# Kernel optimization log

Hardware: AMD Instinct MI355X
Metric: run time of the kernel (lower is better)

## Reference

```python
import jax, jax.numpy as jnp
import numpy as np

U, I, E, T = 60000, 30000, 64, 2000
N = U + I
ADJ_NNZ = 1_600_000
UI_NNZ = 800_000
TAGS_PER_ITEM = 4


def setup_inputs() -> dict:
    key = jax.random.key(0)
    ks = jax.random.split(key, 8)
    # LightGCN normalized adjacency in COO form (values already normalized offline)
    adj_rows = jax.random.randint(ks[0], (ADJ_NNZ,), 0, N, dtype=jnp.int32)
    adj_cols = jax.random.randint(ks[1], (ADJ_NNZ,), 0, N, dtype=jnp.int32)
    adj_vals = jax.random.uniform(ks[2], (ADJ_NNZ,), dtype=jnp.float32) * 0.01
    # Item-tag incidence H: 4 distinct tags per item (binary incidence, no duplicates)
    items_np = np.repeat(np.arange(I, dtype=np.int32), TAGS_PER_ITEM)
    tags_np = ((np.arange(I, dtype=np.int64)[:, None] * 7919 + np.arange(TAGS_PER_ITEM)[None, :] * 131) % T).astype(np.int32).reshape(-1)
    h_items = jnp.asarray(items_np)
    h_tags = jnp.asarray(tags_np)
    # Row-normalized user-item interaction matrix (D_u^-1 @ trn_mat) in COO form
    ui_rows = jax.random.randint(ks[3], (UI_NNZ,), 0, U, dtype=jnp.int32)
    ui_cols = jax.random.randint(ks[4], (UI_NNZ,), 0, I, dtype=jnp.int32)
    ui_vals = jax.random.uniform(ks[5], (UI_NNZ,), dtype=jnp.float32) * 0.01
    return {
        'user_embeds': jax.random.normal(ks[6], (U, E), dtype=jnp.float32) * 0.1,
        'item_embeds': jax.random.normal(jax.random.fold_in(ks[6], 1), (I, E), dtype=jnp.float32) * 0.1,
        'hypergraph_user_embeds': jax.random.normal(ks[7], (U, E), dtype=jnp.float32) * 0.1,
        'hypergraph_item_embeds': jax.random.normal(jax.random.fold_in(ks[7], 1), (I, E), dtype=jnp.float32) * 0.1,
        'adj_rows': adj_rows, 'adj_cols': adj_cols, 'adj_vals': adj_vals,
        'h_items': h_items, 'h_tags': h_tags,
        'ui_rows': ui_rows, 'ui_cols': ui_cols, 'ui_vals': ui_vals,
        'layer_num': 3,
    }


def _spmm(rows, cols, vals, x, n):
    # y[r] += vals[e] * x[cols[e]] for each edge e with rows[e]==r  (t.spmm)
    return jax.ops.segment_sum(vals[:, None] * x[cols], rows, num_segments=n)


def reference(user_embeds, item_embeds, hypergraph_user_embeds, hypergraph_item_embeds,
              adj_rows, adj_cols, adj_vals, h_items, h_tags, ui_rows, ui_cols, ui_vals,
              layer_num):
    ones = jnp.ones(h_items.shape[0], dtype=user_embeds.dtype)
    # B: hyperedge (tag) degree; D: item degree; zero degrees clamped to 1
    B = jax.ops.segment_sum(ones, h_tags, num_segments=T)
    D = jax.ops.segment_sum(ones, h_items, num_segments=I)
    B_inv = 1.0 / jnp.where(B == 0, 1.0, B)
    D_inv = 1.0 / jnp.where(D == 0, 1.0, D)

    def hconv(x):  # D^-1 H B^-1 H^T x, never materializing the item x item adjacency
        y = jax.ops.segment_sum(x[h_items], h_tags, num_segments=T) * B_inv[:, None]
        z = jax.ops.segment_sum(y[h_tags], h_items, num_segments=I)
        return z * D_inv[:, None]

    # LightGCN propagation: sum of all layer embeddings (layer 0 included)
    cur = jnp.concatenate([user_embeds, item_embeds], axis=0)  # [N, E]
    acc = cur
    for _ in range(layer_num):
        cur = _spmm(adj_rows, adj_cols, adj_vals, cur, N)
        acc = acc + cur

    # Hypergraph propagation on items
    hcur = hypergraph_item_embeds
    hacc = hcur
    for _ in range(layer_num):
        hcur = hconv(hcur)
        hacc = hacc + hcur

    # Hypergraph user embeds: own params + degree-normalized sum of interacted items
    hg_user = hypergraph_user_embeds + _spmm(ui_rows, ui_cols, ui_vals, hacc, U)

    return acc[:U], acc[U:], hg_user, hacc
```

## Files before the change

### kernel.cpp

```cpp
#include <hip/hip_runtime.h>

#define E 64
#define TQ 16
#define RPB 256
#define RPB_SHIFT 8
#define NBMAX 1024
#define CHUNK_C 4096
#define CHUNK_P 4096
#define FP8_SCALE 512.0f
#define FP8_INV   (1.0f / 512.0f)

static inline int nblk(long n, int bs) { return (int)((n + bs - 1) / bs); }


__device__ __forceinline__ unsigned short f2bf(float f) {
    unsigned u = __float_as_uint(f);
    u += 0x7FFF + ((u >> 16) & 1);
    return (unsigned short)(u >> 16);
}
__device__ __forceinline__ int f2v15(float f) {
    unsigned u = __float_as_uint(f);
    u += 0x7FFF + ((u >> 16) & 1);
    return (int)((u >> 16) & 0x7FFF);
}
__device__ __forceinline__ float v15f(int p) {
    return __uint_as_float(((unsigned)p >> 17) << 16);
}
__device__ __forceinline__ int pack_fp8x4(float4 v) {
    int w = __builtin_amdgcn_cvt_pk_fp8_f32(v.x, v.y, 0, false);
    w = __builtin_amdgcn_cvt_pk_fp8_f32(v.z, v.w, w, true);
    return w;
}


__global__ void __launch_bounds__(512)
k_count_cvt(const int* __restrict__ adj_rows, int nadj,
            const int* __restrict__ ui_rows, int nui,
            const int* __restrict__ h_tags,
            int* __restrict__ bucket_cnt, int OFF_UI, int OFF_TAG, int NB, int ET,
            const float4* __restrict__ ua, const float4* __restrict__ ub,
            int splitv4, int* __restrict__ xf8, int ncvt, int CB) {
    __shared__ int h4[4][NBMAX];
    if ((int)blockIdx.x < CB) {
        for (int b = threadIdx.x; b < 4 * NBMAX; b += 512) ((int*)h4)[b] = 0;
        __syncthreads();
        int c = (threadIdx.x >> 4) & 3;
        int start = blockIdx.x * CHUNK_C;
        int end = start + CHUNK_C; if (end > ET) end = ET;
        for (int i = start + (int)threadIdx.x; i < end; i += 512) {
            int row;
            if (i < nadj) row = adj_rows[i];
            else if (i < nadj + nui) row = OFF_UI + ui_rows[i - nadj];
            else row = OFF_TAG + h_tags[i - nadj - nui];
            atomicAdd(&h4[c][row >> RPB_SHIFT], 1);
        }
        __syncthreads();
        for (int b = threadIdx.x; b < NB; b += 512) {
            int tot = h4[0][b] + h4[1][b] + h4[2][b] + h4[3][b];
            if (tot) atomicAdd(&bucket_cnt[b], tot);
        }
    } else {
        int i = ((int)blockIdx.x - CB) * 512 + threadIdx.x;
        if (i < ncvt) {
            float4 v = (i < splitv4) ? ua[i] : ub[i - splitv4];
            v.x *= FP8_SCALE; v.y *= FP8_SCALE; v.z *= FP8_SCALE; v.w *= FP8_SCALE;
            xf8[i] = pack_fp8x4(v);
        }
    }
}


__global__ void __launch_bounds__(1024)
k_scan_nb(const int* __restrict__ cnt, int* __restrict__ base, int* __restrict__ bcur,
          int* __restrict__ rp, int M, int NB, int ET) {
    __shared__ int sh[1024];
    int tid = threadIdx.x;
    int v = (tid < NB) ? cnt[tid] : 0;
    sh[tid] = v;
    __syncthreads();
    for (int off = 1; off < 1024; off <<= 1) {
        int t = (tid >= off) ? sh[tid - off] : 0;
        __syncthreads();
        sh[tid] += t;
        __syncthreads();
    }
    if (tid < NB) {
        int excl = sh[tid] - v;
        base[tid] = excl;
        bcur[tid] = excl;
        if (tid == NB - 1) base[NB] = sh[tid];
    }
    if (tid == 0) rp[M] = ET;
}


__global__ void __launch_bounds__(512)
k_partition(const int* __restrict__ adj_rows, const int* __restrict__ adj_cols,
            const float* __restrict__ adj_vals, int nadj,
            const int* __restrict__ ui_rows, const int* __restrict__ ui_cols,
            const float* __restrict__ ui_vals, int nui,
            const int* __restrict__ h_tags, const int* __restrict__ h_items,
            int* __restrict__ bcur, int2* __restrict__ staged,
            int OFF_UI, int OFF_TAG, int NB, int ET) {
    __shared__ int h4[4][NBMAX];
    for (int b = threadIdx.x; b < 4 * NBMAX; b += 512) ((int*)h4)[b] = 0;
    __syncthreads();

    int c = (threadIdx.x >> 4) & 3;
    int start = blockIdx.x * CHUNK_P;

    int rowA[8], colA[8], vbA[8];
    #pragma unroll
    for (int k = 0; k < 8; ++k) {
        int i = start + k * 512 + (int)threadIdx.x;
        int row = -1, col = 0, vb = 0;
        if (i < ET) {
            if (i < nadj) {
                row = adj_rows[i]; col = adj_cols[i]; vb = f2v15(adj_vals[i]);
            } else if (i < nadj + nui) {
                int j = i - nadj;
                row = OFF_UI + ui_rows[j]; col = ui_cols[j]; vb = f2v15(ui_vals[j]);
            } else {
                int j = i - nadj - nui;
                row = OFF_TAG + h_tags[j]; col = h_items[j]; vb = 0;
            }
            atomicAdd(&h4[c][row >> RPB_SHIFT], 1);
        }
        rowA[k] = row; colA[k] = col; vbA[k] = vb;
    }
    __syncthreads();

    for (int b = threadIdx.x; b < NB; b += 512) {
        int c0 = h4[0][b], c1 = h4[1][b], c2 = h4[2][b], c3 = h4[3][b];
        int tot = c0 + c1 + c2 + c3;
        if (tot) {
            int g = atomicAdd(&bcur[b], tot);
            h4[0][b] = g;
            h4[1][b] = g + c0;
            h4[2][b] = g + c0 + c1;
            h4[3][b] = g + c0 + c1 + c2;
        }
    }
    __syncthreads();

    #pragma unroll
    for (int k = 0; k < 8; ++k) {
        if (rowA[k] >= 0) {
            int b = rowA[k] >> RPB_SHIFT;
            int pos = atomicAdd(&h4[c][b], 1);
            staged[pos] = make_int2(((rowA[k] & (RPB - 1)) << 17) | colA[k], vbA[k]);
        }
    }
}


__global__ void __launch_bounds__(512)
k_bucket_csr(const int2* __restrict__ staged, const int* __restrict__ bbase,
             int* __restrict__ rp, int* __restrict__ pool, int M,
             int OFF_UI, int OFF_TAG) {
    __shared__ int h4[4][1024];
    __shared__ int scn[1024];
    int b = blockIdx.x;
    int s0 = bbase[b], s1 = bbase[b + 1];
    int row0 = b << RPB_SHIFT;
    int shift = (row0 >= OFF_TAG) ? 13 : ((row0 >= OFF_UI) ? 14 : 15);
    int tid = threadIdx.x;
    for (int i = tid; i < 4 * 1024; i += 512) ((int*)h4)[i] = 0;
    __syncthreads();
    int c = (tid >> 4) & 3;
    for (int e = s0 + tid; e < s1; e += 512) {
        int w = staged[e].x;
        int lrow = ((unsigned)w) >> 17;
        int col = w & 0x1FFFF;
        int qb = col >> shift; if (qb > 3) qb = 3;
        atomicAdd(&h4[c][(lrow << 2) | qb], 1);
    }
    __syncthreads();
    int k0 = tid, k1 = tid + 512;
    int tot0 = h4[0][k0] + h4[1][k0] + h4[2][k0] + h4[3][k0];
    int tot1 = h4[0][k1] + h4[1][k1] + h4[2][k1] + h4[3][k1];
    scn[k0] = tot0; scn[k1] = tot1;
    __syncthreads();
    for (int off = 1; off < 1024; off <<= 1) {
        int a0 = (k0 >= off) ? scn[k0 - off] : 0;
        int a1 = (k1 >= off) ? scn[k1 - off] : 0;
        __syncthreads();
        scn[k0] += a0; scn[k1] += a1;
        __syncthreads();
    }
    {
        int excl0 = s0 + scn[k0] - tot0;
        int excl1 = s0 + scn[k1] - tot1;
        if ((k0 & 3) == 0) { int r = row0 + (k0 >> 2); if (r < M) rp[r] = excl0; }
        if ((k1 & 3) == 0) { int r = row0 + (k1 >> 2); if (r < M) rp[r] = excl1; }
        int c00 = h4[0][k0], c10 = h4[1][k0], c20 = h4[2][k0];
        h4[0][k0] = excl0;
        h4[1][k0] = excl0 + c00;
        h4[2][k0] = excl0 + c00 + c10;
        h4[3][k0] = excl0 + c00 + c10 + c20;
        int c01 = h4[0][k1], c11 = h4[1][k1], c21 = h4[2][k1];
        h4[0][k1] = excl1;
        h4[1][k1] = excl1 + c01;
        h4[2][k1] = excl1 + c01 + c11;
        h4[3][k1] = excl1 + c01 + c11 + c21;
    }
    __syncthreads();
    for (int e = s0 + tid; e < s1; e += 512) {
        int2 ed = staged[e];
        int lrow = ((unsigned)ed.x) >> 17;
        int col = ed.x & 0x1FFFF;
        int qb = col >> shift; if (qb > 3) qb = 3;
        int pos = atomicAdd(&h4[c][(lrow << 2) | qb], 1);
        pool[pos] = (ed.y << 17) | col;
    }
}


#define FP8_ACC2(sa, sb, wx, wy, vv)                                      \
    sa.x += vv * __builtin_amdgcn_cvt_f32_fp8(wx, 0);                     \
    sa.y += vv * __builtin_amdgcn_cvt_f32_fp8(wx, 1);                     \
    sa.z += vv * __builtin_amdgcn_cvt_f32_fp8(wx, 2);                     \
    sa.w += vv * __builtin_amdgcn_cvt_f32_fp8(wx, 3);                     \
    sb.x += vv * __builtin_amdgcn_cvt_f32_fp8(wy, 0);                     \
    sb.y += vv * __builtin_amdgcn_cvt_f32_fp8(wy, 1);                     \
    sb.z += vv * __builtin_amdgcn_cvt_f32_fp8(wy, 2);                     \
    sb.w += vv * __builtin_amdgcn_cvt_f32_fp8(wy, 3);

struct f8acc { float4 a, b; };

__device__ __forceinline__ f8acc spmm8_sum(const int* __restrict__ pool,
                                           const int2* __restrict__ xf2,
                                           int s0, int s1, int q) {
    float4 sa = make_float4(0.f, 0.f, 0.f, 0.f);
    float4 sb = make_float4(0.f, 0.f, 0.f, 0.f);
    int e = s0;
    for (; e + 8 <= s1; e += 8) {
        int p0 = pool[e],     p1 = pool[e + 1], p2 = pool[e + 2], p3 = pool[e + 3];
        int p4 = pool[e + 4], p5 = pool[e + 5], p6 = pool[e + 6], p7 = pool[e + 7];
        int2 w0 = xf2[(long)(p0 & 0x1FFFF) * 8 + q];
        int2 w1 = xf2[(long)(p1 & 0x1FFFF) * 8 + q];
        int2 w2 = xf2[(long)(p2 & 0x1FFFF) * 8 + q];
        int2 w3 = xf2[(long)(p3 & 0x1FFFF) * 8 + q];
        int2 w4 = xf2[(long)(p4 & 0x1FFFF) * 8 + q];
        int2 w5 = xf2[(long)(p5 & 0x1FFFF) * 8 + q];
        int2 w6 = xf2[(long)(p6 & 0x1FFFF) * 8 + q];
        int2 w7 = xf2[(long)(p7 & 0x1FFFF) * 8 + q];
        FP8_ACC2(sa, sb, w0.x, w0.y, v15f(p0));
        FP8_ACC2(sa, sb, w1.x, w1.y, v15f(p1));
        FP8_ACC2(sa, sb, w2.x, w2.y, v15f(p2));
        FP8_ACC2(sa, sb, w3.x, w3.y, v15f(p3));
        FP8_ACC2(sa, sb, w4.x, w4.y, v15f(p4));
        FP8_ACC2(sa, sb, w5.x, w5.y, v15f(p5));
        FP8_ACC2(sa, sb, w6.x, w6.y, v15f(p6));
        FP8_ACC2(sa, sb, w7.x, w7.y, v15f(p7));
    }
    for (; e + 4 <= s1; e += 4) {
        int p0 = pool[e], p1 = pool[e + 1], p2 = pool[e + 2], p3 = pool[e + 3];
        int2 w0 = xf2[(long)(p0 & 0x1FFFF) * 8 + q];
        int2 w1 = xf2[(long)(p1 & 0x1FFFF) * 8 + q];
        int2 w2 = xf2[(long)(p2 & 0x1FFFF) * 8 + q];
        int2 w3 = xf2[(long)(p3 & 0x1FFFF) * 8 + q];
        FP8_ACC2(sa, sb, w0.x, w0.y, v15f(p0));
        FP8_ACC2(sa, sb, w1.x, w1.y, v15f(p1));
        FP8_ACC2(sa, sb, w2.x, w2.y, v15f(p2));
        FP8_ACC2(sa, sb, w3.x, w3.y, v15f(p3));
    }
    for (; e < s1; ++e) {
        int p0 = pool[e];
        int2 w0 = xf2[(long)(p0 & 0x1FFFF) * 8 + q];
        FP8_ACC2(sa, sb, w0.x, w0.y, v15f(p0));
    }
    f8acc r; r.a = sa; r.b = sb;
    return r;
}

__device__ __forceinline__ void spmm8_body(const int* __restrict__ rp,
                                           const int* __restrict__ pool,
                                           const int2* __restrict__ xf2,
                                           int2* __restrict__ yf2, int n, int bid) {
    int gid = bid * 256 + (int)threadIdx.x;
    int row = gid >> 3;
    if (row >= n) return;
    int q = gid & 7;
    f8acc s = spmm8_sum(pool, xf2, rp[row], rp[row + 1], q);
    int2 o;
    o.x = pack_fp8x4(s.a);
    o.y = pack_fp8x4(s.b);
    yf2[(long)row * 8 + q] = o;
}

__device__ __forceinline__ void spmm8_acc_body(const int* __restrict__ rp,
                                               const int* __restrict__ pool,
                                               const int2* __restrict__ xf2,
                                               const int2* __restrict__ l1,
                                               const int2* __restrict__ l2,
                                               const float4* __restrict__ ua,
                                               const float4* __restrict__ ub,
                                               int splitv4, float4* __restrict__ acc,
                                               int n, int bid) {
    int gid = bid * 256 + (int)threadIdx.x;
    int row = gid >> 3;
    if (row >= n) return;
    int q = gid & 7;
    f8acc s = spmm8_sum(pool, xf2, rp[row], rp[row + 1], q);
    long i0 = (long)row * 16 + q * 2;
    float4 a0 = (i0 < splitv4) ? ua[i0] : ub[i0 - splitv4];
    float4 a1 = (i0 + 1 < splitv4) ? ua[i0 + 1] : ub[i0 + 1 - splitv4];
    int2 w1 = l1[(long)row * 8 + q];
    int2 w2 = l2[(long)row * 8 + q];
    a0.x += (__builtin_amdgcn_cvt_f32_fp8(w1.x, 0) + __builtin_amdgcn_cvt_f32_fp8(w2.x, 0)
             + s.a.x) * FP8_INV;
    a0.y += (__builtin_amdgcn_cvt_f32_fp8(w1.x, 1) + __builtin_amdgcn_cvt_f32_fp8(w2.x, 1)
             + s.a.y) * FP8_INV;
    a0.z += (__builtin_amdgcn_cvt_f32_fp8(w1.x, 2) + __builtin_amdgcn_cvt_f32_fp8(w2.x, 2)
             + s.a.z) * FP8_INV;
    a0.w += (__builtin_amdgcn_cvt_f32_fp8(w1.x, 3) + __builtin_amdgcn_cvt_f32_fp8(w2.x, 3)
             + s.a.w) * FP8_INV;
    a1.x += (__builtin_amdgcn_cvt_f32_fp8(w1.y, 0) + __builtin_amdgcn_cvt_f32_fp8(w2.y, 0)
             + s.b.x) * FP8_INV;
    a1.y += (__builtin_amdgcn_cvt_f32_fp8(w1.y, 1) + __builtin_amdgcn_cvt_f32_fp8(w2.y, 1)
             + s.b.y) * FP8_INV;
    a1.z += (__builtin_amdgcn_cvt_f32_fp8(w1.y, 2) + __builtin_amdgcn_cvt_f32_fp8(w2.y, 2)
             + s.b.z) * FP8_INV;
    a1.w += (__builtin_amdgcn_cvt_f32_fp8(w1.y, 3) + __builtin_amdgcn_cvt_f32_fp8(w2.y, 3)
             + s.b.w) * FP8_INV;
    acc[i0] = a0;
    acc[i0 + 1] = a1;
}

__device__ __forceinline__ void tag_hop_body(const int* __restrict__ rp, int rp_off,
                                             const int* __restrict__ pool,
                                             const float* __restrict__ x,
                                             float* __restrict__ y, int ntags, int bid) {
    int t = (bid * 256 + (int)threadIdx.x) >> 6;
    if (t >= ntags) return;
    int lane = threadIdx.x & 63;
    int q = lane & 15;
    int g = lane >> 4;
    int s0 = rp[rp_off + t], s1 = rp[rp_off + t + 1];
    float4 s = make_float4(0.f, 0.f, 0.f, 0.f);
    for (int e = s0 + g; e < s1; e += 4) {
        int it = pool[e] & 0x1FFFF;
        float4 xv = ((const float4*)x)[(long)it * TQ + q];
        s.x += xv.x; s.y += xv.y; s.z += xv.z; s.w += xv.w;
    }
    s.x += __shfl_xor(s.x, 16, 64); s.y += __shfl_xor(s.y, 16, 64);
    s.z += __shfl_xor(s.z, 16, 64); s.w += __shfl_xor(s.w, 16, 64);
    s.x += __shfl_xor(s.x, 32, 64); s.y += __shfl_xor(s.y, 32, 64);
    s.z += __shfl_xor(s.z, 32, 64); s.w += __shfl_xor(s.w, 32, 64);
    if (g == 0) {
        int b = s1 - s0;
        float binv = (b > 0) ? (1.f / (float)b) : 1.f;
        s.x *= binv; s.y *= binv; s.z *= binv; s.w *= binv;
        ((float4*)y)[(long)t * TQ + q] = s;
    }
}

__device__ __forceinline__ void tag_g_body(const int* __restrict__ rp, int rp_off,
                                           const int* __restrict__ pool,
                                           const int* __restrict__ tags, int K,
                                           const float* __restrict__ yin,
                                           const float* __restrict__ yprev,
                                           float* __restrict__ yout, int ntags, int bid) {
    int t = (bid * 256 + (int)threadIdx.x) >> 6;
    if (t >= ntags) return;
    int lane = threadIdx.x & 63;
    int q = lane & 15;
    int g = lane >> 4;
    int s0 = rp[rp_off + t], s1 = rp[rp_off + t + 1];
    float4 s = make_float4(0.f, 0.f, 0.f, 0.f);
    if (K == 4) {
        for (int e = s0 + g; e < s1; e += 4) {
            int it = pool[e] & 0x1FFFF;
            int4 t4 = ((const int4*)tags)[it];
            float4 a0 = ((const float4*)yin)[(long)t4.x * TQ + q];
            float4 a1 = ((const float4*)yin)[(long)t4.y * TQ + q];
            float4 a2 = ((const float4*)yin)[(long)t4.z * TQ + q];
            float4 a3 = ((const float4*)yin)[(long)t4.w * TQ + q];
            s.x += (a0.x + a1.x) + (a2.x + a3.x);
            s.y += (a0.y + a1.y) + (a2.y + a3.y);
            s.z += (a0.z + a1.z) + (a2.z + a3.z);
            s.w += (a0.w + a1.w) + (a2.w + a3.w);
        }
    } else {
        for (int e = s0 + g; e < s1; e += 4) {
            int it = pool[e] & 0x1FFFF;
            for (int k = 0; k < K; ++k) {
                int tt = tags[(long)it * K + k];
                float4 a = ((const float4*)yin)[(long)tt * TQ + q];
                s.x += a.x; s.y += a.y; s.z += a.z; s.w += a.w;
            }
        }
    }
    s.x += __shfl_xor(s.x, 16, 64); s.y += __shfl_xor(s.y, 16, 64);
    s.z += __shfl_xor(s.z, 16, 64); s.w += __shfl_xor(s.w, 16, 64);
    s.x += __shfl_xor(s.x, 32, 64); s.y += __shfl_xor(s.y, 32, 64);
    s.z += __shfl_xor(s.z, 32, 64); s.w += __shfl_xor(s.w, 32, 64);
    if (g == 0) {
        int b = s1 - s0;
        float dinv = 1.f / (float)K;
        float f = (b > 0) ? (dinv / (float)b) : 0.f;
        s.x *= f; s.y *= f; s.z *= f; s.w *= f;
        long o = (long)t * TQ + q;
        if (yprev) {
            float4 p1 = ((const float4*)yprev)[o];
            float4 p2 = ((const float4*)yin)[o];
            s.x += p1.x + p2.x; s.y += p1.y + p2.y;
            s.z += p1.z + p2.z; s.w += p1.w + p2.w;
        }
        ((float4*)yout)[o] = s;
    }
}


__global__ void __launch_bounds__(256)
k_spmm_tag(const int* __restrict__ rp, const int* __restrict__ pool,
           const int2* __restrict__ xf2, int2* __restrict__ yf2, int n, int SB,
           int rp_off, const float* __restrict__ xtag, float* __restrict__ y1,
           int ntags) {
    if ((int)blockIdx.x < SB)
        spmm8_body(rp, pool, xf2, yf2, n, blockIdx.x);
    else
        tag_hop_body(rp, rp_off, pool, xtag, y1, ntags, (int)blockIdx.x - SB);
}

__global__ void __launch_bounds__(256)
k_spmm_g(const int* __restrict__ rp, const int* __restrict__ pool,
         const int2* __restrict__ xf2, int2* __restrict__ yf2, int n, int SB,
         int rp_off, const int* __restrict__ tags, int K,
         const float* __restrict__ yin, const float* __restrict__ yprev,
         float* __restrict__ yout, int ntags) {
    if ((int)blockIdx.x < SB)
        spmm8_body(rp, pool, xf2, yf2, n, blockIdx.x);
    else
        tag_g_body(rp, rp_off, pool, tags, K, yin, yprev, yout, ntags,
                   (int)blockIdx.x - SB);
}

__global__ void __launch_bounds__(256)
k_spmm_final(const int* __restrict__ rp, const int* __restrict__ pool,
             const int2* __restrict__ xf2, const int2* __restrict__ l1,
             const int2* __restrict__ l2,
             const float4* __restrict__ ua, const float4* __restrict__ ub,
             int splitv4, float4* __restrict__ acc, int n, int SB,
             int rp_off, const int* __restrict__ tags, int K,
             const float* __restrict__ yin, const float* __restrict__ yprev,
             float* __restrict__ yout, int ntags) {
    if ((int)blockIdx.x < SB)
        spmm8_acc_body(rp, pool, xf2, l1, l2, ua, ub, splitv4, acc, n, blockIdx.x);
    else
        tag_g_body(rp, rp_off, pool, tags, K, yin, yprev, yout, ntags,
                   (int)blockIdx.x - SB);
}

__global__ void __launch_bounds__(256)
k_items(const int* __restrict__ tags, int K, const float* __restrict__ ysum,
        const float* __restrict__ init, float* __restrict__ hacc,
        ushort4* __restrict__ hacc_bf, int nitems) {
    int gid = blockIdx.x * 256 + (int)threadIdx.x;
    int i = gid >> 4;
    if (i >= nitems) return;
    int q = gid & 15;
    float4 s = make_float4(0.f, 0.f, 0.f, 0.f);
    if (K == 4) {
        int4 t4 = ((const int4*)tags)[i];
        float4 y0 = ((const float4*)ysum)[(long)t4.x * TQ + q];
        float4 y1 = ((const float4*)ysum)[(long)t4.y * TQ + q];
        float4 y2 = ((const float4*)ysum)[(long)t4.z * TQ + q];
        float4 y3 = ((const float4*)ysum)[(long)t4.w * TQ + q];
        s.x = (y0.x + y1.x) + (y2.x + y3.x);
        s.y = (y0.y + y1.y) + (y2.y + y3.y);
        s.z = (y0.z + y1.z) + (y2.z + y3.z);
        s.w = (y0.w + y1.w) + (y2.w + y3.w);
    } else {
        for (int k = 0; k < K; ++k) {
            int tt = tags[(long)i * K + k];
            float4 yv = ((const float4*)ysum)[(long)tt * TQ + q];
            s.x += yv.x; s.y += yv.y; s.z += yv.z; s.w += yv.w;
        }
    }
    float dinv = 1.f / (float)K;
    s.x *= dinv; s.y *= dinv; s.z *= dinv; s.w *= dinv;
    long o = (long)i * TQ + q;
    float4 a = ((const float4*)init)[o];
    a.x += s.x; a.y += s.y; a.z += s.z; a.w += s.w;
    ((float4*)hacc)[o] = a;
    ushort4 hb;
    hb.x = f2bf(a.x); hb.y = f2bf(a.y); hb.z = f2bf(a.z); hb.w = f2bf(a.w);
    hacc_bf[o] = hb;
}


#define BF_ACC2(sa, sb, hv, vv)                                           \
    sa.x += vv * __uint_as_float(hv.x << 16);                             \
    sa.y += vv * __uint_as_float(hv.x & 0xFFFF0000u);                     \
    sa.z += vv * __uint_as_float(hv.y << 16);                             \
    sa.w += vv * __uint_as_float(hv.y & 0xFFFF0000u);                     \
    sb.x += vv * __uint_as_float(hv.z << 16);                             \
    sb.y += vv * __uint_as_float(hv.z & 0xFFFF0000u);                     \
    sb.z += vv * __uint_as_float(hv.w << 16);                             \
    sb.w += vv * __uint_as_float(hv.w & 0xFFFF0000u);

__global__ void __launch_bounds__(256)
k_csr_spmm_base_bf(const int* __restrict__ rp, int rp_off,
                   const int* __restrict__ pool,
                   const uint4* __restrict__ xbf,
                   const float4* __restrict__ base,
                   float4* __restrict__ out, int n) {
    int gid = blockIdx.x * 256 + (int)threadIdx.x;
    int row = gid >> 3;
    if (row >= n) return;
    int q = gid & 7;
    int s0 = rp[rp_off + row], s1 = rp[rp_off + row + 1];
    float4 sa = make_float4(0.f, 0.f, 0.f, 0.f);
    float4 sb = make_float4(0.f, 0.f, 0.f, 0.f);
    int e = s0;
    for (; e + 8 <= s1; e += 8) {
        int p0 = pool[e],     p1 = pool[e + 1], p2 = pool[e + 2], p3 = pool[e + 3];
        int p4 = pool[e + 4], p5 = pool[e + 5], p6 = pool[e + 6], p7 = pool[e + 7];
        uint4 h0 = xbf[(long)(p0 & 0x1FFFF) * 8 + q];
        uint4 h1 = xbf[(long)(p1 & 0x1FFFF) * 8 + q];
        uint4 h2 = xbf[(long)(p2 & 0x1FFFF) * 8 + q];
        uint4 h3 = xbf[(long)(p3 & 0x1FFFF) * 8 + q];
        uint4 h4 = xbf[(long)(p4 & 0x1FFFF) * 8 + q];
        uint4 h5 = xbf[(long)(p5 & 0x1FFFF) * 8 + q];
        uint4 h6 = xbf[(long)(p6 & 0x1FFFF) * 8 + q];
        uint4 h7 = xbf[(long)(p7 & 0x1FFFF) * 8 + q];
        BF_ACC2(sa, sb, h0, v15f(p0)); BF_ACC2(sa, sb, h1, v15f(p1));
        BF_ACC2(sa, sb, h2, v15f(p2)); BF_ACC2(sa, sb, h3, v15f(p3));
        BF_ACC2(sa, sb, h4, v15f(p4)); BF_ACC2(sa, sb, h5, v15f(p5));
        BF_ACC2(sa, sb, h6, v15f(p6)); BF_ACC2(sa, sb, h7, v15f(p7));
    }
    for (; e + 4 <= s1; e += 4) {
        int p0 = pool[e], p1 = pool[e + 1], p2 = pool[e + 2], p3 = pool[e + 3];
        uint4 h0 = xbf[(long)(p0 & 0x1FFFF) * 8 + q];
        uint4 h1 = xbf[(long)(p1 & 0x1FFFF) * 8 + q];
        uint4 h2 = xbf[(long)(p2 & 0x1FFFF) * 8 + q];
        uint4 h3 = xbf[(long)(p3 & 0x1FFFF) * 8 + q];
        BF_ACC2(sa, sb, h0, v15f(p0)); BF_ACC2(sa, sb, h1, v15f(p1));
        BF_ACC2(sa, sb, h2, v15f(p2)); BF_ACC2(sa, sb, h3, v15f(p3));
    }
    for (; e < s1; ++e) {
        int p0 = pool[e];
        uint4 h0 = xbf[(long)(p0 & 0x1FFFF) * 8 + q];
        BF_ACC2(sa, sb, h0, v15f(p0));
    }
    long o = (long)row * 16 + q * 2;
    float4 b0 = base[o];
    float4 b1 = base[o + 1];
    b0.x += sa.x; b0.y += sa.y; b0.z += sa.z; b0.w += sa.w;
    b1.x += sb.x; b1.y += sb.y; b1.z += sb.z; b1.w += sb.w;
    out[o] = b0;
    out[o + 1] = b1;
}


extern "C" void kernel_launch(void* const* d_in, const int* in_sizes, int n_in,
                              void* d_out, int out_size, void* d_ws, size_t ws_size,
                              hipStream_t stream) {
    const float* user_embeds = (const float*)d_in[0];
    const float* item_embeds = (const float*)d_in[1];
    const float* hyper_user  = (const float*)d_in[2];
    const float* hyper_item  = (const float*)d_in[3];
    const int*   adj_rows    = (const int*)d_in[4];
    const int*   adj_cols    = (const int*)d_in[5];
    const float* adj_vals    = (const float*)d_in[6];
    const int*   h_items     = (const int*)d_in[7];
    const int*   h_tags      = (const int*)d_in[8];
    const int*   ui_rows     = (const int*)d_in[9];
    const int*   ui_cols     = (const int*)d_in[10];
    const float* ui_vals     = (const float*)d_in[11];

    const int U = in_sizes[0] / E;
    const int I = in_sizes[1] / E;
    const int N = U + I;
    const int ADJ = in_sizes[4];
    const int NH  = in_sizes[7];
    const int UI  = in_sizes[9];
    const int K   = NH / I;
    const int T   = 2000;
    const int ET  = ADJ + UI + NH;

    const int OFF_UI  = (N + RPB - 1) & ~(RPB - 1);
    const int OFF_TAG = (OFF_UI + U + RPB - 1) & ~(RPB - 1);
    const int M   = OFF_TAG + T;
    const int NB  = (M + RPB - 1) >> RPB_SHIFT;

    float* out     = (float*)d_out;
    float* acc     = out;
    float* hg_user = out + (size_t)N * E;
    float* hacc    = hg_user + (size_t)U * E;

    char* ws = (char*)d_ws;
    auto alloc = [&](size_t bytes) { char* p = ws; ws += (bytes + 255) & ~(size_t)255; return p; };

    int*  xf0 = (int*)alloc((size_t)N * TQ * sizeof(int));
    int*  xf1 = (int*)alloc((size_t)N * TQ * sizeof(int));
    int*  xf2 = (int*)alloc((size_t)N * TQ * sizeof(int));
    int2* staged = (int2*)alloc((size_t)ET * sizeof(int2));
    float* y1      = (float*)alloc((size_t)T * E * sizeof(float));
    float* y2      = (float*)alloc((size_t)T * E * sizeof(float));
    float* ys      = (float*)alloc((size_t)T * E * sizeof(float));
    unsigned short* hacc_bf = (unsigned short*)alloc((size_t)I * E * sizeof(unsigned short));
    int*   pool    = (int*)alloc((size_t)ET * sizeof(int));
    int*   rp      = (int*)alloc((size_t)(M + 1) * sizeof(int));
    int*   bcnt    = (int*)alloc((size_t)NBMAX * sizeof(int));
    int*   bbase   = (int*)alloc((size_t)(NBMAX + 1) * sizeof(int));
    int*   bcur    = (int*)alloc((size_t)NBMAX * sizeof(int));

    const int BS = 256;
    const int TAG_BLOCKS = nblk((long)T * 64, 256);
    const int CB  = nblk(ET, CHUNK_C);
    const int CVB = nblk((long)N * TQ, 512);
    const int SB8 = nblk((long)N * 8, BS);
    const int IB  = nblk((long)I * TQ, BS);

    hipMemsetAsync(bcnt, 0, (size_t)NB * sizeof(int), stream);
    k_count_cvt<<<CB + CVB, 512, 0, stream>>>(
        adj_rows, ADJ, ui_rows, UI, h_tags, bcnt, OFF_UI, OFF_TAG, NB, ET,
        (const float4*)user_embeds, (const float4*)item_embeds, U * TQ,
        xf0, N * TQ, CB);
    k_scan_nb<<<1, 1024, 0, stream>>>(bcnt, bbase, bcur, rp, M, NB, ET);
    k_partition<<<nblk(ET, CHUNK_P), 512, 0, stream>>>(
        adj_rows, adj_cols, adj_vals, ADJ, ui_rows, ui_cols, ui_vals, UI,
        h_tags, h_items, bcur, staged, OFF_UI, OFF_TAG, NB, ET);
    k_bucket_csr<<<NB, 512, 0, stream>>>(staged, bbase, rp, pool, M, OFF_UI, OFF_TAG);

    k_spmm_tag<<<SB8 + TAG_BLOCKS, BS, 0, stream>>>(
        rp, pool, (const int2*)xf0, (int2*)xf1, N, SB8, OFF_TAG, hyper_item, y1, T);
    k_spmm_g<<<SB8 + TAG_BLOCKS, BS, 0, stream>>>(
        rp, pool, (const int2*)xf1, (int2*)xf2, N, SB8, OFF_TAG, h_tags, K,
        y1, nullptr, y2, T);
    k_spmm_final<<<SB8 + TAG_BLOCKS, BS, 0, stream>>>(
        rp, pool, (const int2*)xf2, (const int2*)xf1, (const int2*)xf2,
        (const float4*)user_embeds, (const float4*)item_embeds, U * TQ,
        (float4*)acc, N, SB8, OFF_TAG, h_tags, K, y2, y1, ys, T);

    k_items<<<IB, BS, 0, stream>>>(
        h_tags, K, ys, hyper_item, hacc, (ushort4*)hacc_bf, I);

    k_csr_spmm_base_bf<<<nblk((long)U * 8, BS), BS, 0, stream>>>(
        rp, OFF_UI, pool, (const uint4*)hacc_bf, (const float4*)hyper_user,
        (float4*)hg_user, U);
}
```

Baseline: 319.9 us.

## Fold bucket scan into partition, unroll SpMM gather to 16, add occupancy bounds

```diff
diff --git a/kernel.cpp b/kernel.cpp
--- a/kernel.cpp
+++ b/kernel.cpp
@@ -70,49 +70,56 @@
 }
 
 
-__global__ void __launch_bounds__(1024)
-k_scan_nb(const int* __restrict__ cnt, int* __restrict__ base, int* __restrict__ bcur,
-          int* __restrict__ rp, int M, int NB, int ET) {
-    __shared__ int sh[1024];
-    int tid = threadIdx.x;
-    int v = (tid < NB) ? cnt[tid] : 0;
-    sh[tid] = v;
-    __syncthreads();
-    for (int off = 1; off < 1024; off <<= 1) {
-        int t = (tid >= off) ? sh[tid - off] : 0;
-        __syncthreads();
-        sh[tid] += t;
-        __syncthreads();
-    }
-    if (tid < NB) {
-        int excl = sh[tid] - v;
-        base[tid] = excl;
-        bcur[tid] = excl;
-        if (tid == NB - 1) base[NB] = sh[tid];
-    }
-    if (tid == 0) rp[M] = ET;
-}
-
-
 __global__ void __launch_bounds__(512)
 k_partition(const int* __restrict__ adj_rows, const int* __restrict__ adj_cols,
             const float* __restrict__ adj_vals, int nadj,
             const int* __restrict__ ui_rows, const int* __restrict__ ui_cols,
             const float* __restrict__ ui_vals, int nui,
             const int* __restrict__ h_tags, const int* __restrict__ h_items,
-            int* __restrict__ bcur, int2* __restrict__ staged,
-            int OFF_UI, int OFF_TAG, int NB, int ET) {
+            const int* __restrict__ bcnt, int* __restrict__ bcur,
+            int* __restrict__ bbase, int* __restrict__ rp,
+            int2* __restrict__ staged,
+            int OFF_UI, int OFF_TAG, int NB, int ET, int M) {
     __shared__ int h4[4][NBMAX];
-    for (int b = threadIdx.x; b < 4 * NBMAX; b += 512) ((int*)h4)[b] = 0;
+    __shared__ int basesh[NBMAX];
+    int tid = (int)threadIdx.x;
+    int k0 = tid, k1 = tid + 512;
+
+    {
+        int* scn = (int*)h4;
+        int v0 = (k0 < NB) ? bcnt[k0] : 0;
+        int v1 = (k1 < NB) ? bcnt[k1] : 0;
+        scn[k0] = v0; scn[k1] = v1;
+        __syncthreads();
+        for (int off = 1; off < 1024; off <<= 1) {
+            int a0 = (k0 >= off) ? scn[k0 - off] : 0;
+            int a1 = (k1 >= off) ? scn[k1 - off] : 0;
+            __syncthreads();
+            scn[k0] += a0; scn[k1] += a1;
+            __syncthreads();
+        }
+        basesh[k0] = scn[k0] - v0;
+        basesh[k1] = scn[k1] - v1;
+        if (blockIdx.x == 0) {
+            if (k0 < NB) bbase[k0] = scn[k0] - v0;
+            if (k1 < NB) bbase[k1] = scn[k1] - v1;
+            if (k0 == NB - 1) bbase[NB] = scn[k0];
+            if (k1 == NB - 1) bbase[NB] = scn[k1];
+            if (tid == 0) rp[M] = ET;
+        }
+        __syncthreads();
+    }
+
+    for (int b = tid; b < 4 * NBMAX; b += 512) ((int*)h4)[b] = 0;
     __syncthreads();
 
-    int c = (threadIdx.x >> 4) & 3;
+    int c = (tid >> 4) & 3;
     int start = blockIdx.x * CHUNK_P;
 
     int rowA[8], colA[8], vbA[8];
     #pragma unroll
     for (int k = 0; k < 8; ++k) {
-        int i = start + k * 512 + (int)threadIdx.x;
+        int i = start + k * 512 + tid;
         int row = -1, col = 0, vb = 0;
         if (i < ET) {
             if (i < nadj) {
@@ -130,11 +137,11 @@
     }
     __syncthreads();
 
-    for (int b = threadIdx.x; b < NB; b += 512) {
+    for (int b = tid; b < NB; b += 512) {
         int c0 = h4[0][b], c1 = h4[1][b], c2 = h4[2][b], c3 = h4[3][b];
         int tot = c0 + c1 + c2 + c3;
         if (tot) {
-            int g = atomicAdd(&bcur[b], tot);
+            int g = basesh[b] + atomicAdd(&bcur[b], tot);
             h4[0][b] = g;
             h4[1][b] = g + c0;
             h4[2][b] = g + c0 + c1;
@@ -234,6 +241,44 @@
     float4 sa = make_float4(0.f, 0.f, 0.f, 0.f);
     float4 sb = make_float4(0.f, 0.f, 0.f, 0.f);
     int e = s0;
+    for (; e + 16 <= s1; e += 16) {
+        int p0 = pool[e],      p1 = pool[e + 1],  p2 = pool[e + 2],  p3 = pool[e + 3];
+        int p4 = pool[e + 4],  p5 = pool[e + 5],  p6 = pool[e + 6],  p7 = pool[e + 7];
+        int p8 = pool[e + 8],  p9 = pool[e + 9],  pa = pool[e + 10], pb = pool[e + 11];
+        int pc = pool[e + 12], pd = pool[e + 13], pe = pool[e + 14], pf = pool[e + 15];
+        int2 w0 = xf2[(long)(p0 & 0x1FFFF) * 8 + q];
+        int2 w1 = xf2[(long)(p1 & 0x1FFFF) * 8 + q];
+        int2 w2 = xf2[(long)(p2 & 0x1FFFF) * 8 + q];
+        int2 w3 = xf2[(long)(p3 & 0x1FFFF) * 8 + q];
+        int2 w4 = xf2[(long)(p4 & 0x1FFFF) * 8 + q];
+        int2 w5 = xf2[(long)(p5 & 0x1FFFF) * 8 + q];
+        int2 w6 = xf2[(long)(p6 & 0x1FFFF) * 8 + q];
+        int2 w7 = xf2[(long)(p7 & 0x1FFFF) * 8 + q];
+        int2 w8 = xf2[(long)(p8 & 0x1FFFF) * 8 + q];
+        int2 w9 = xf2[(long)(p9 & 0x1FFFF) * 8 + q];
+        int2 wa = xf2[(long)(pa & 0x1FFFF) * 8 + q];
+        int2 wb = xf2[(long)(pb & 0x1FFFF) * 8 + q];
+        int2 wc = xf2[(long)(pc & 0x1FFFF) * 8 + q];
+        int2 wd = xf2[(long)(pd & 0x1FFFF) * 8 + q];
+        int2 we = xf2[(long)(pe & 0x1FFFF) * 8 + q];
+        int2 wf = xf2[(long)(pf & 0x1FFFF) * 8 + q];
+        FP8_ACC2(sa, sb, w0.x, w0.y, v15f(p0));
+        FP8_ACC2(sa, sb, w1.x, w1.y, v15f(p1));
+        FP8_ACC2(sa, sb, w2.x, w2.y, v15f(p2));
+        FP8_ACC2(sa, sb, w3.x, w3.y, v15f(p3));
+        FP8_ACC2(sa, sb, w4.x, w4.y, v15f(p4));
+        FP8_ACC2(sa, sb, w5.x, w5.y, v15f(p5));
+        FP8_ACC2(sa, sb, w6.x, w6.y, v15f(p6));
+        FP8_ACC2(sa, sb, w7.x, w7.y, v15f(p7));
+        FP8_ACC2(sa, sb, w8.x, w8.y, v15f(p8));
+        FP8_ACC2(sa, sb, w9.x, w9.y, v15f(p9));
+        FP8_ACC2(sa, sb, wa.x, wa.y, v15f(pa));
+        FP8_ACC2(sa, sb, wb.x, wb.y, v15f(pb));
+        FP8_ACC2(sa, sb, wc.x, wc.y, v15f(pc));
+        FP8_ACC2(sa, sb, wd.x, wd.y, v15f(pd));
+        FP8_ACC2(sa, sb, we.x, we.y, v15f(pe));
+        FP8_ACC2(sa, sb, wf.x, wf.y, v15f(pf));
+    }
     for (; e + 8 <= s1; e += 8) {
         int p0 = pool[e],     p1 = pool[e + 1], p2 = pool[e + 2], p3 = pool[e + 3];
         int p4 = pool[e + 4], p5 = pool[e + 5], p6 = pool[e + 6], p7 = pool[e + 7];
@@ -413,7 +458,7 @@
 }
 
 
-__global__ void __launch_bounds__(256)
+__global__ void __launch_bounds__(256, 4)
 k_spmm_tag(const int* __restrict__ rp, const int* __restrict__ pool,
            const int2* __restrict__ xf2, int2* __restrict__ yf2, int n, int SB,
            int rp_off, const float* __restrict__ xtag, float* __restrict__ y1,
@@ -424,7 +469,7 @@
         tag_hop_body(rp, rp_off, pool, xtag, y1, ntags, (int)blockIdx.x - SB);
 }
 
-__global__ void __launch_bounds__(256)
+__global__ void __launch_bounds__(256, 4)
 k_spmm_g(const int* __restrict__ rp, const int* __restrict__ pool,
          const int2* __restrict__ xf2, int2* __restrict__ yf2, int n, int SB,
          int rp_off, const int* __restrict__ tags, int K,
@@ -437,7 +482,7 @@
                    (int)blockIdx.x - SB);
 }
 
-__global__ void __launch_bounds__(256)
+__global__ void __launch_bounds__(256, 4)
 k_spmm_final(const int* __restrict__ rp, const int* __restrict__ pool,
              const int2* __restrict__ xf2, const int2* __restrict__ l1,
              const int2* __restrict__ l2,
@@ -604,9 +649,9 @@
     unsigned short* hacc_bf = (unsigned short*)alloc((size_t)I * E * sizeof(unsigned short));
     int*   pool    = (int*)alloc((size_t)ET * sizeof(int));
     int*   rp      = (int*)alloc((size_t)(M + 1) * sizeof(int));
-    int*   bcnt    = (int*)alloc((size_t)NBMAX * sizeof(int));
+    int*   bcnt    = (int*)alloc((size_t)2 * NBMAX * sizeof(int));
+    int*   bcur    = bcnt + NBMAX;
     int*   bbase   = (int*)alloc((size_t)(NBMAX + 1) * sizeof(int));
-    int*   bcur    = (int*)alloc((size_t)NBMAX * sizeof(int));
 
     const int BS = 256;
     const int TAG_BLOCKS = nblk((long)T * 64, 256);
@@ -615,15 +660,14 @@
     const int SB8 = nblk((long)N * 8, BS);
     const int IB  = nblk((long)I * TQ, BS);
 
-    hipMemsetAsync(bcnt, 0, (size_t)NB * sizeof(int), stream);
+    hipMemsetAsync(bcnt, 0, (size_t)2 * NBMAX * sizeof(int), stream);
     k_count_cvt<<<CB + CVB, 512, 0, stream>>>(
         adj_rows, ADJ, ui_rows, UI, h_tags, bcnt, OFF_UI, OFF_TAG, NB, ET,
         (const float4*)user_embeds, (const float4*)item_embeds, U * TQ,
         xf0, N * TQ, CB);
-    k_scan_nb<<<1, 1024, 0, stream>>>(bcnt, bbase, bcur, rp, M, NB, ET);
     k_partition<<<nblk(ET, CHUNK_P), 512, 0, stream>>>(
         adj_rows, adj_cols, adj_vals, ADJ, ui_rows, ui_cols, ui_vals, UI,
-        h_tags, h_items, bcur, staged, OFF_UI, OFF_TAG, NB, ET);
+        h_tags, h_items, bcnt, bcur, bbase, rp, staged, OFF_UI, OFF_TAG, NB, ET, M);
     k_bucket_csr<<<NB, 512, 0, stream>>>(staged, bbase, rp, pool, M, OFF_UI, OFF_TAG);
 
     k_spmm_tag<<<SB8 + TAG_BLOCKS, BS, 0, stream>>>(
```

New measurement: 317.0 us. Within noise of the previous version (-0.9%).
